# Kernel optimization log

Hardware: AMD Instinct MI355X
Metric: run time of the kernel (lower is better)

The kernel has to match this reference:

```python
import jax, jax.numpy as jnp
import numpy as np

N, F, H, G = 4096, 256, 8, 128  # atoms, filters, heads, groups
D = F // H  # head dim = 32


def setup_inputs() -> dict:
    key = jax.random.key(0)
    ks = jax.random.split(key, 12)
    x = jax.random.normal(ks[0], (N, F), dtype=jnp.float32)
    # sorted group ids in [0, G): block_diag over unique-count blocks == equality mask on sorted ids
    seg = jnp.sort(jax.random.randint(ks[1], (N,), 0, G, dtype=jnp.int32))
    elem_index = jnp.stack([jnp.arange(N, dtype=jnp.int32), seg])  # [2, N]
    s = 1.0 / np.sqrt(F)
    def lin(k):
        kw, kb = jax.random.split(k)
        return (jax.random.normal(kw, (F, F), dtype=jnp.float32) * s,
                jnp.zeros((F,), dtype=jnp.float32))
    Wq, bq = lin(ks[2]); Wk, bk = lin(ks[3]); Wv, bv = lin(ks[4])
    Wo1, bo1 = lin(ks[5]); Wo2, bo2 = lin(ks[6])
    return {"x": x, "elem_index": elem_index,
            "Wq": Wq, "bq": bq, "Wk": Wk, "bk": bk, "Wv": Wv, "bv": bv,
            "Wo1": Wo1, "bo1": bo1, "Wo2": Wo2, "bo2": bo2}


def reference(x, elem_index, Wq, bq, Wk, bk, Wv, bv, Wo1, bo1, Wo2, bo2):
    n = x.shape[0]
    # projections -> [H, N, D]
    q = (x @ Wq.T + bq).reshape(n, H, D).transpose(1, 0, 2)
    k = (x @ Wk.T + bk).reshape(n, H, D).transpose(1, 0, 2)
    v = (x @ Wv.T + bv).reshape(n, H, D).transpose(1, 0, 2)
    attn = jnp.einsum('hnd,hmd->hnm', q, k)          # [H, N, N]
    attn = jax.nn.silu(attn)                          # attn_act = activation() in source
    seg = elem_index[1]
    mask = (seg[:, None] == seg[None, :]).astype(attn.dtype)  # block-diagonal (sorted ids)
    attn = attn * mask
    out = jnp.einsum('hnm,hmd->hnd', attn, v)        # [H, N, D]
    out = out.transpose(1, 0, 2).reshape(n, F)       # [N, F]
    out = out @ Wo1.T + bo1
    out = jax.ops.segment_sum(out, seg, num_segments=G)  # scatter sum by group -> [G, F]
    out = out @ Wo2.T + bo2
    return jax.nn.silu(out)
```

## Files before the change

kernel.cpp:

```cpp
#include <hip/hip_runtime.h>
#include <math.h>

#define NATOMS 4096
#define FDIM   256
#define NHEAD  8
#define DHEAD  32
#define NGRP   128

__device__ __forceinline__ float silu_f(float x) {
    return x / (1.0f + __expf(-x));
}

__global__ void offsets_kernel(const int* __restrict__ seg,
                               int* __restrict__ off,
                               float* __restrict__ cntf) {
    int g = threadIdx.x;
    if (g >= NGRP) return;
    auto lb = [&](int val) {
        int lo = 0, hi = NATOMS;
        while (lo < hi) {
            int mid = (lo + hi) >> 1;
            if (seg[mid] < val) lo = mid + 1; else hi = mid;
        }
        return lo;
    };
    int a = lb(g);
    int b = lb(g + 1);
    off[g] = a;
    if (g == NGRP - 1) off[NGRP] = NATOMS;
    cntf[g] = (float)(b - a);
}

__global__ __launch_bounds__(256) void gemm_qkv(
    const float* __restrict__ A,
    const float* __restrict__ W0, const float* __restrict__ W1, const float* __restrict__ W2,
    const float* __restrict__ b0, const float* __restrict__ b1, const float* __restrict__ b2,
    float* __restrict__ C0, float* __restrict__ C1, float* __restrict__ C2)
{
    const int K = FDIM, Ncols = FDIM;
    __shared__ float As[16][68];
    __shared__ float Bs[3][16][68];

    int tid = threadIdx.x;
    int bm = blockIdx.y * 64;
    int bn = blockIdx.x * 64;
    int tx = tid & 15;
    int ty = tid >> 4;
    int lm = tid >> 2;
    int lk = (tid & 3) << 2;

    const float* Ws[3] = {W0, W1, W2};

    float acc[3][4][4] = {};

    for (int kt = 0; kt < K; kt += 16) {
        const float4 av = *(const float4*)(A + (size_t)(bm + lm) * K + kt + lk);
        As[lk + 0][lm] = av.x; As[lk + 1][lm] = av.y;
        As[lk + 2][lm] = av.z; As[lk + 3][lm] = av.w;
#pragma unroll
        for (int w = 0; w < 3; ++w) {
            const float4 bv = *(const float4*)(Ws[w] + (size_t)(bn + lm) * K + kt + lk);
            Bs[w][lk + 0][lm] = bv.x; Bs[w][lk + 1][lm] = bv.y;
            Bs[w][lk + 2][lm] = bv.z; Bs[w][lk + 3][lm] = bv.w;
        }
        __syncthreads();

#pragma unroll
        for (int kk = 0; kk < 16; ++kk) {
            float4 a = *(const float4*)&As[kk][ty * 4];
            float4 b[3];
#pragma unroll
            for (int w = 0; w < 3; ++w) b[w] = *(const float4*)&Bs[w][kk][tx * 4];
            float ar[4] = {a.x, a.y, a.z, a.w};
#pragma unroll
            for (int w = 0; w < 3; ++w) {
                float br[4] = {b[w].x, b[w].y, b[w].z, b[w].w};
#pragma unroll
                for (int i = 0; i < 4; ++i)
#pragma unroll
                    for (int j = 0; j < 4; ++j)
                        acc[w][i][j] = fmaf(ar[i], br[j], acc[w][i][j]);
            }
        }
        __syncthreads();
    }

    float* Cs[3] = {C0, C1, C2};
    const float* bs[3] = {b0, b1, b2};
#pragma unroll
    for (int w = 0; w < 3; ++w) {
#pragma unroll
        for (int i = 0; i < 4; ++i) {
            int m = bm + ty * 4 + i;
#pragma unroll
            for (int j = 0; j < 4; ++j) {
                int n = bn + tx * 4 + j;
                Cs[w][(size_t)m * Ncols + n] = acc[w][i][j] + bs[w][n];
            }
        }
    }
}

__global__ __launch_bounds__(256) void gemm_small(
    const float* __restrict__ A, const float* __restrict__ B,
    const float* __restrict__ bias, const float* __restrict__ rowScale,
    float* __restrict__ C, int M, int Ncols, int K, int act)
{
    __shared__ float As[32][36];
    __shared__ float Bs[32][36];

    int tid = threadIdx.x;
    int bm = blockIdx.y * 32;
    int bn = blockIdx.x * 32;
    int tx = tid & 15;
    int ty = tid >> 4;
    int lm = tid >> 3;
    int lk = (tid & 7) << 2;

    float acc[2][2] = {};

    for (int kt = 0; kt < K; kt += 32) {
        const float4 av = *(const float4*)(A + (size_t)(bm + lm) * K + kt + lk);
        const float4 bv = *(const float4*)(B + (size_t)(bn + lm) * K + kt + lk);
        As[lk + 0][lm] = av.x; As[lk + 1][lm] = av.y;
        As[lk + 2][lm] = av.z; As[lk + 3][lm] = av.w;
        Bs[lk + 0][lm] = bv.x; Bs[lk + 1][lm] = bv.y;
        Bs[lk + 2][lm] = bv.z; Bs[lk + 3][lm] = bv.w;
        __syncthreads();

#pragma unroll
        for (int kk = 0; kk < 32; ++kk) {
            float a0 = As[kk][ty * 2], a1 = As[kk][ty * 2 + 1];
            float c0 = Bs[kk][tx * 2], c1 = Bs[kk][tx * 2 + 1];
            acc[0][0] = fmaf(a0, c0, acc[0][0]);
            acc[0][1] = fmaf(a0, c1, acc[0][1]);
            acc[1][0] = fmaf(a1, c0, acc[1][0]);
            acc[1][1] = fmaf(a1, c1, acc[1][1]);
        }
        __syncthreads();
    }

#pragma unroll
    for (int i = 0; i < 2; ++i) {
        int m = bm + ty * 2 + i;
        float rs = rowScale ? rowScale[m] : 1.0f;
#pragma unroll
        for (int j = 0; j < 2; ++j) {
            int n = bn + tx * 2 + j;
            float vv = acc[i][j] + rs * bias[n];
            if (act) vv = silu_f(vv);
            C[(size_t)m * Ncols + n] = vv;
        }
    }
}

#define JT 32
#define IT 64

__global__ __launch_bounds__(256) void attn_kernel(
    const float* __restrict__ q, const float* __restrict__ k,
    const float* __restrict__ v, const int* __restrict__ off,
    float* __restrict__ Ysum)
{
    int g = blockIdx.x, h = blockIdx.y;
    int base = off[g];
    int n = off[g + 1] - base;

    __shared__ float4 qt4[IT * 8];
    __shared__ float4 vt4[JT * 8];
    __shared__ float  wred[8][JT];
    __shared__ float  w[JT];
    __shared__ float  red[8][DHEAD];

    int tid = threadIdx.x;
    int jj = tid & 31;
    int iq = tid >> 5;
    int d = tid & 31;
    int r = tid >> 5;

    const float4* q4 = (const float4*)(q + (size_t)base * FDIM) + h * 8;
    const float4* k4 = (const float4*)(k + (size_t)base * FDIM) + h * 8;
    const float4* v4 = (const float4*)(v + (size_t)base * FDIM) + h * 8;

    float accY = 0.0f;

    for (int j0 = 0; j0 < n; j0 += JT) {
        int jt_n = min(JT, n - j0);
        __syncthreads();
        for (int idx = tid; idx < jt_n * 8; idx += 256)
            vt4[idx] = v4[(size_t)(j0 + (idx >> 3)) * 64 + (idx & 7)];

        float4 kr[8];
        {
            int jrow = (jj < jt_n) ? (j0 + jj) : j0;
#pragma unroll
            for (int c = 0; c < 8; ++c) kr[c] = k4[(size_t)jrow * 64 + c];
        }

        float wpart = 0.0f;
        for (int i0 = 0; i0 < n; i0 += IT) {
            int it_n = min(IT, n - i0);
            __syncthreads();
            for (int idx = tid; idx < it_n * 8; idx += 256)
                qt4[idx] = q4[(size_t)(i0 + (idx >> 3)) * 64 + (idx & 7)];
            __syncthreads();
            if (jj < jt_n) {
                for (int ii = iq; ii < it_n; ii += 8) {
                    const float4* qr = &qt4[ii * 8];
                    float s = 0.0f;
#pragma unroll
                    for (int c = 0; c < 8; ++c) {
                        float4 a = qr[c];
                        s = fmaf(a.x, kr[c].x, s);
                        s = fmaf(a.y, kr[c].y, s);
                        s = fmaf(a.z, kr[c].z, s);
                        s = fmaf(a.w, kr[c].w, s);
                    }
                    wpart += silu_f(s);
                }
            }
        }
        wred[iq][jj] = wpart;
        __syncthreads();
        if (tid < JT) {
            float s = 0.0f;
#pragma unroll
            for (int rr = 0; rr < 8; ++rr) s += wred[rr][tid];
            w[tid] = s;
        }
        __syncthreads();
        const float* vts = (const float*)vt4;
        for (int j = r; j < jt_n; j += 8)
            accY = fmaf(w[j], vts[j * 32 + d], accY);
    }

    red[r][d] = accY;
    __syncthreads();
    if (r == 0) {
        float s = 0.0f;
#pragma unroll
        for (int rr = 0; rr < 8; ++rr) s += red[rr][d];
        Ysum[(size_t)g * FDIM + h * DHEAD + d] = s;
    }
}

extern "C" void kernel_launch(void* const* d_in, const int* in_sizes, int n_in,
                              void* d_out, int out_size, void* d_ws, size_t ws_size,
                              hipStream_t stream) {
    const float* x    = (const float*)d_in[0];
    const int*   eidx = (const int*)  d_in[1];
    const float* Wq   = (const float*)d_in[2];
    const float* bq   = (const float*)d_in[3];
    const float* Wk   = (const float*)d_in[4];
    const float* bk   = (const float*)d_in[5];
    const float* Wv   = (const float*)d_in[6];
    const float* bv   = (const float*)d_in[7];
    const float* Wo1  = (const float*)d_in[8];
    const float* bo1  = (const float*)d_in[9];
    const float* Wo2  = (const float*)d_in[10];
    const float* bo2  = (const float*)d_in[11];
    float* out = (float*)d_out;

    const int* seg = eidx + NATOMS;

    const size_t NF = (size_t)NATOMS * FDIM;
    const size_t GF = (size_t)NGRP * FDIM;
    float* q    = (float*)d_ws;
    float* k    = q + NF;
    float* v    = k + NF;
    float* Ysum = v + NF;
    float* S    = Ysum + GF;
    float* cntf = S + GF;
    int*   off  = (int*)(cntf + NGRP);

    offsets_kernel<<<1, 128, 0, stream>>>(seg, off, cntf);

    dim3 gproj(FDIM / 64, NATOMS / 64);
    gemm_qkv<<<gproj, 256, 0, stream>>>(x, Wq, Wk, Wv, bq, bk, bv, q, k, v);

    dim3 gattn(NGRP, NHEAD);
    attn_kernel<<<gattn, 256, 0, stream>>>(q, k, v, off, Ysum);

    dim3 gsmall(FDIM / 32, NGRP / 32);
    gemm_small<<<gsmall, 256, 0, stream>>>(Ysum, Wo1, bo1, cntf, S, NGRP, FDIM, FDIM, 0);

    gemm_small<<<gsmall, 256, 0, stream>>>(S, Wo2, bo2, nullptr, out, NGRP, FDIM, FDIM, 1);
}
```

Before: 146.3 us.

## Convert QKV projection to bf16 MFMA with fused prep and offsets kernel

Adds a prep kernel that converts x and the three projection weights to bf16, concatenates the biases, and computes the group offsets, replacing the separate offsets kernel. The fp32 shared-memory SIMT QKV GEMM becomes a bf16 MFMA 16x16x32 kernel that reads operands straight from global memory into registers and writes q, k and v with bias added. The aim is to use matrix cores for the projection. In exchange it lowers precision to bf16 and adds a conversion pass over x and the weights on every call. It also clamps the attention segment bounds.

Result: faster. 128.2 us (-12.4%).

```diff
diff --git a/kernel.cpp b/kernel.cpp
--- a/kernel.cpp
+++ b/kernel.cpp
@@ -7,95 +7,123 @@
 #define DHEAD  32
 #define NGRP   128
 
+typedef __bf16 bf16x8 __attribute__((ext_vector_type(8)));
+typedef float  floatx4 __attribute__((ext_vector_type(4)));
+typedef unsigned short u16x4 __attribute__((ext_vector_type(4)));
+
 __device__ __forceinline__ float silu_f(float x) {
     return x / (1.0f + __expf(-x));
 }
 
-__global__ void offsets_kernel(const int* __restrict__ seg,
-                               int* __restrict__ off,
-                               float* __restrict__ cntf) {
-    int g = threadIdx.x;
-    if (g >= NGRP) return;
-    auto lb = [&](int val) {
-        int lo = 0, hi = NATOMS;
-        while (lo < hi) {
-            int mid = (lo + hi) >> 1;
-            if (seg[mid] < val) lo = mid + 1; else hi = mid;
-        }
-        return lo;
-    };
-    int a = lb(g);
-    int b = lb(g + 1);
-    off[g] = a;
-    if (g == NGRP - 1) off[NGRP] = NATOMS;
-    cntf[g] = (float)(b - a);
-}
-
-__global__ __launch_bounds__(256) void gemm_qkv(
-    const float* __restrict__ A,
-    const float* __restrict__ W0, const float* __restrict__ W1, const float* __restrict__ W2,
-    const float* __restrict__ b0, const float* __restrict__ b1, const float* __restrict__ b2,
-    float* __restrict__ C0, float* __restrict__ C1, float* __restrict__ C2)
+__device__ __forceinline__ unsigned short f2bf(float f) {
+    union { float f; unsigned int u; } a;
+    a.f = f;
+    unsigned int r = a.u + 0x7FFF + ((a.u >> 16) & 1);
+    return (unsigned short)(r >> 16);
+}
+
+__global__ __launch_bounds__(256) void prep_kernel(
+    const float* __restrict__ x,
+    const float* __restrict__ Wq, const float* __restrict__ Wk, const float* __restrict__ Wv,
+    const float* __restrict__ bq, const float* __restrict__ bk, const float* __restrict__ bv,
+    const int* __restrict__ seg,
+    unsigned short* __restrict__ xb, unsigned short* __restrict__ Wb,
+    float* __restrict__ b_all, int* __restrict__ off, float* __restrict__ cntf)
 {
-    const int K = FDIM, Ncols = FDIM;
-    __shared__ float As[16][68];
-    __shared__ float Bs[3][16][68];
-
     int tid = threadIdx.x;
-    int bm = blockIdx.y * 64;
-    int bn = blockIdx.x * 64;
-    int tx = tid & 15;
-    int ty = tid >> 4;
-    int lm = tid >> 2;
-    int lk = (tid & 3) << 2;
-
-    const float* Ws[3] = {W0, W1, W2};
-
-    float acc[3][4][4] = {};
-
-    for (int kt = 0; kt < K; kt += 16) {
-        const float4 av = *(const float4*)(A + (size_t)(bm + lm) * K + kt + lk);
-        As[lk + 0][lm] = av.x; As[lk + 1][lm] = av.y;
-        As[lk + 2][lm] = av.z; As[lk + 3][lm] = av.w;
-#pragma unroll
-        for (int w = 0; w < 3; ++w) {
-            const float4 bv = *(const float4*)(Ws[w] + (size_t)(bn + lm) * K + kt + lk);
-            Bs[w][lk + 0][lm] = bv.x; Bs[w][lk + 1][lm] = bv.y;
-            Bs[w][lk + 2][lm] = bv.z; Bs[w][lk + 3][lm] = bv.w;
-        }
-        __syncthreads();
-
-#pragma unroll
-        for (int kk = 0; kk < 16; ++kk) {
-            float4 a = *(const float4*)&As[kk][ty * 4];
-            float4 b[3];
-#pragma unroll
-            for (int w = 0; w < 3; ++w) b[w] = *(const float4*)&Bs[w][kk][tx * 4];
-            float ar[4] = {a.x, a.y, a.z, a.w};
-#pragma unroll
-            for (int w = 0; w < 3; ++w) {
-                float br[4] = {b[w].x, b[w].y, b[w].z, b[w].w};
-#pragma unroll
-                for (int i = 0; i < 4; ++i)
-#pragma unroll
-                    for (int j = 0; j < 4; ++j)
-                        acc[w][i][j] = fmaf(ar[i], br[j], acc[w][i][j]);
+    unsigned int u = blockIdx.x * 256 + tid;
+
+    if (blockIdx.x == 0 && tid < NGRP) {
+        int g = tid;
+        auto lb = [&](int val) {
+            int lo = 0, hi = NATOMS;
+            while (lo < hi) {
+                int mid = (lo + hi) >> 1;
+                if (seg[mid] < val) lo = mid + 1; else hi = mid;
             }
-        }
-        __syncthreads();
-    }
-
-    float* Cs[3] = {C0, C1, C2};
-    const float* bs[3] = {b0, b1, b2};
-#pragma unroll
-    for (int w = 0; w < 3; ++w) {
-#pragma unroll
-        for (int i = 0; i < 4; ++i) {
-            int m = bm + ty * 4 + i;
-#pragma unroll
-            for (int j = 0; j < 4; ++j) {
-                int n = bn + tx * 4 + j;
-                Cs[w][(size_t)m * Ncols + n] = acc[w][i][j] + bs[w][n];
+            return lo;
+        };
+        int a = lb(g);
+        int b = lb(g + 1);
+        off[g] = a;
+        if (g == NGRP - 1) off[NGRP] = NATOMS;
+        cntf[g] = (float)(b - a);
+    }
+    if (blockIdx.x == 1 && tid < 192) {
+        const float* src = (tid < 64) ? bq : (tid < 128) ? bk : bv;
+        int t = tid & 63;
+        ((float4*)b_all)[tid] = ((const float4*)src)[t];
+    }
+
+    const unsigned int NX4 = 262144;
+    const unsigned int NW4 = 16384;
+    float4 fv;
+    u16x4* dst;
+    if (u < NX4) {
+        fv = ((const float4*)x)[u];
+        dst = (u16x4*)xb + u;
+    } else {
+        unsigned int r = u - NX4;
+        unsigned int w = r / NW4;
+        unsigned int i = r - w * NW4;
+        const float* W = (w == 0) ? Wq : (w == 1) ? Wk : Wv;
+        fv = ((const float4*)W)[i];
+        dst = (u16x4*)Wb + (size_t)w * NW4 + i;
+    }
+    u16x4 o;
+    o[0] = f2bf(fv.x); o[1] = f2bf(fv.y); o[2] = f2bf(fv.z); o[3] = f2bf(fv.w);
+    *dst = o;
+}
+
+__global__ __launch_bounds__(256) void qkv_mfma(
+    const unsigned short* __restrict__ xb, const unsigned short* __restrict__ Wb,
+    const float* __restrict__ b_all, float* __restrict__ qkv)
+{
+    int tid = threadIdx.x;
+    int lane = tid & 63;
+    int ww = tid >> 6;
+    int wrow = ww >> 1, wcol = ww & 1;
+    int m_base = blockIdx.x * 64 + wrow * 32;
+    int n_base = blockIdx.y * 128 + wcol * 64;
+
+    int l15 = lane & 15;
+    int quad = lane >> 4;
+    int kq = quad * 8;
+
+    floatx4 acc[2][4] = {};
+
+    const unsigned short* arow0 = xb + (size_t)(m_base + l15) * 256 + kq;
+    const unsigned short* arow1 = arow0 + 16 * 256;
+    const unsigned short* brow[4];
+#pragma unroll
+    for (int ni = 0; ni < 4; ++ni)
+        brow[ni] = Wb + (size_t)(n_base + ni * 16 + l15) * 256 + kq;
+
+#pragma unroll
+    for (int ks = 0; ks < 8; ++ks) {
+        int ko = ks * 32;
+        bf16x8 a0 = *(const bf16x8*)(arow0 + ko);
+        bf16x8 a1 = *(const bf16x8*)(arow1 + ko);
+#pragma unroll
+        for (int ni = 0; ni < 4; ++ni) {
+            bf16x8 b = *(const bf16x8*)(brow[ni] + ko);
+            acc[0][ni] = __builtin_amdgcn_mfma_f32_16x16x32_bf16(a0, b, acc[0][ni], 0, 0, 0);
+            acc[1][ni] = __builtin_amdgcn_mfma_f32_16x16x32_bf16(a1, b, acc[1][ni], 0, 0, 0);
+        }
+    }
+
+#pragma unroll
+    for (int mi = 0; mi < 2; ++mi) {
+#pragma unroll
+        for (int ni = 0; ni < 4; ++ni) {
+            int col_g = n_base + ni * 16 + l15;
+            int w = col_g >> 8, c = col_g & 255;
+            float bias = b_all[col_g];
+            float* outp = qkv + (size_t)w * (NATOMS * FDIM) + c;
+#pragma unroll
+            for (int r = 0; r < 4; ++r) {
+                int row = m_base + mi * 16 + quad * 4 + r;
+                outp[(size_t)row * FDIM] = acc[mi][ni][r] + bias;
             }
         }
     }
@@ -164,7 +192,10 @@
 {
     int g = blockIdx.x, h = blockIdx.y;
     int base = off[g];
-    int n = off[g + 1] - base;
+    int end  = off[g + 1];
+    base = min(max(base, 0), NATOMS);
+    end  = min(max(end, base), NATOMS);
+    int n = end - base;
 
     __shared__ float4 qt4[IT * 8];
     __shared__ float4 vt4[JT * 8];
@@ -265,18 +296,23 @@
 
     const size_t NF = (size_t)NATOMS * FDIM;
     const size_t GF = (size_t)NGRP * FDIM;
-    float* q    = (float*)d_ws;
-    float* k    = q + NF;
-    float* v    = k + NF;
-    float* Ysum = v + NF;
-    float* S    = Ysum + GF;
-    float* cntf = S + GF;
-    int*   off  = (int*)(cntf + NGRP);
-
-    offsets_kernel<<<1, 128, 0, stream>>>(seg, off, cntf);
-
-    dim3 gproj(FDIM / 64, NATOMS / 64);
-    gemm_qkv<<<gproj, 256, 0, stream>>>(x, Wq, Wk, Wv, bq, bk, bv, q, k, v);
+
+    float* q     = (float*)d_ws;
+    float* k     = q + NF;
+    float* v     = k + NF;
+    float* Ysum  = v + NF;
+    float* S     = Ysum + GF;
+    float* cntf  = S + GF;
+    float* b_all = cntf + NGRP;
+    int*   off   = (int*)(b_all + 768);
+    unsigned short* xb = (unsigned short*)((float*)off + 160);
+    unsigned short* Wb = xb + NF;
+
+    prep_kernel<<<1216, 256, 0, stream>>>(x, Wq, Wk, Wv, bq, bk, bv, seg,
+                                          xb, Wb, b_all, off, cntf);
+
+    dim3 gproj(NATOMS / 64, 768 / 128);
+    qkv_mfma<<<gproj, 256, 0, stream>>>(xb, Wb, b_all, q);
 
     dim3 gattn(NGRP, NHEAD);
     attn_kernel<<<gattn, 256, 0, stream>>>(q, k, v, off, Ysum);
```
